# Performance work log

Measured on AMD Instinct MI355X. Metric: run time of the kernel, lower is better.

The kernel has to match this reference:

```python
import jax, jax.numpy as jnp
import numpy as np

B, N, E = 64, 128, 512
F_NODE, F_EDGE = 16, 8
NODE_SIZE = EDGE_SIZE = 64
NUM_STEPS, N_ITER, OMEGA = 3, 8, 0.75
CUTOFF, SMEAR, EPS = 50.0, -0.39, 1e-6


def mila(x):
    # mila with beta=-1: x * tanh(softplus(x - 1))
    return x * jnp.tanh(jax.nn.softplus(x - 1.0))


def ssp(x):
    return jax.nn.softplus(x) + 1e-3


def setup_inputs():
    key = jax.random.key(0)
    ks = iter(jax.random.split(key, 64))
    def nrm(shape, s=1.0):
        return jax.random.normal(next(ks), shape, jnp.float32) * s
    def he(shape):
        return nrm(shape, (2.0 / shape[-2]) ** 0.5)
    inp = {}
    inp['nodes1'] = nrm((N, F_NODE))
    inp['edges1'] = nrm((E, F_EDGE))
    inp['senders1'] = jax.random.randint(next(ks), (E,), 0, N)
    inp['receivers1'] = jax.random.randint(next(ks), (E,), 0, N)
    inp['nodes2'] = nrm((N, F_NODE))
    inp['edges2'] = nrm((E, F_EDGE))
    inp['senders2'] = jax.random.randint(next(ks), (E,), 0, N)
    inp['receivers2'] = jax.random.randint(next(ks), (E,), 0, N)
    c1 = jax.random.uniform(next(ks), (B, N, 3), jnp.float32, 0.0, 10.0)
    c2 = jax.random.uniform(next(ks), (B, N, 3), jnp.float32, 0.0, 10.0) + jnp.array([12.0, 0.0, 0.0])
    inp['coords1'], inp['coords2'] = c1, c2
    inp['distance_matrices'] = jnp.linalg.norm(c1[:, :, None, :] - c2[:, None, :, :], axis=-1)
    inp['multipoles'] = nrm((2, B, N, 1), 0.2)
    inp['W_emb_node'], inp['b_emb_node'] = he((F_NODE, NODE_SIZE)), jnp.zeros((NODE_SIZE,))
    inp['W_emb_edge'], inp['b_emb_edge'] = he((F_EDGE, EDGE_SIZE)), jnp.zeros((EDGE_SIZE,))
    inp['W_gn_edge'] = he((NUM_STEPS, EDGE_SIZE + 2 * NODE_SIZE, EDGE_SIZE))
    inp['b_gn_edge'] = jnp.zeros((NUM_STEPS, EDGE_SIZE))
    inp['W_gn_node'] = he((NUM_STEPS, NODE_SIZE + EDGE_SIZE, NODE_SIZE))
    inp['b_gn_node'] = jnp.zeros((NUM_STEPS, NODE_SIZE))
    inp['pp_W0'], inp['pp_b0'] = he((2 * NODE_SIZE, NODE_SIZE)), jnp.zeros((NODE_SIZE,))
    inp['pp_W1'], inp['pp_b1'] = he((NODE_SIZE, NODE_SIZE)), jnp.zeros((NODE_SIZE,))
    inp['pp_W2'], inp['pp_b2'] = he((NODE_SIZE, 5)), jnp.zeros((5,))
    inp['ap_W0'], inp['ap_b0'] = he((NODE_SIZE, NODE_SIZE)), jnp.zeros((NODE_SIZE,))
    inp['ap_W1'], inp['ap_b1'] = he((NODE_SIZE, NODE_SIZE)), jnp.zeros((NODE_SIZE,))
    inp['ap_W2'], inp['ap_b2'] = he((NODE_SIZE, 5)), jnp.zeros((5,))
    return inp


def _gnn(nodes, edges, senders, receivers, Wen, ben, Wee, bee, Wge, bge, Wgn, bgn):
    # GraphIndependent embedding, then NUM_STEPS InteractionNetwork blocks
    n = mila(nodes @ Wen + ben)
    e = mila(edges @ Wee + bee)
    for s in range(NUM_STEPS):
        e_in = jnp.concatenate([e, n[receivers], n[senders]], axis=-1)
        e = mila(e_in @ Wge[s] + bge[s])
        agg = jax.ops.segment_sum(e, receivers, num_segments=N)
        n = mila(jnp.concatenate([n, agg], axis=-1) @ Wgn[s] + bgn[s])
    return n


def _mlp3(x, W0, b0, W1, b1, W2, b2):
    h = mila(x @ W0 + b0)
    h = mila(h @ W1 + b1)
    return ssp(h @ W2 + b2)


def _induction(coords1, coords2, pol1, pol2, dist, q1, q2):
    # Thole-damped SCF induced dipoles between the two monomers
    r12 = coords1[:, :, None, :] - coords2[:, None, :, :]            # [B,N,N,3]
    R = dist[..., None]                                              # [B,N,N,1]
    R3 = R ** 3 + EPS
    au = jnp.sqrt(pol1[:, 0][:, None] * pol2[:, 0][None, :]) + EPS   # [N,N]
    u3 = dist ** 3 / au                                              # [B,N,N]
    exu = jnp.exp(SMEAR * u3)
    lam3 = (1.0 - exu)[..., None]
    lam5 = (1.0 - (1.0 - SMEAR * u3) * exu)[..., None]
    E0_1 = jnp.sum(q2[:, None, :, None] * lam3 * r12 / R3, axis=2)   # [B,N,3]
    E0_2 = jnp.sum(q1[:, :, None, None] * lam3 * (-r12) / R3, axis=1)
    eye = jnp.eye(3, dtype=coords1.dtype)
    T12 = (3.0 * lam5[..., None] * r12[..., :, None] * r12[..., None, :] / (R ** 5 + EPS)[..., None]
           - lam3[..., None] * eye / R3[..., None])                  # [B,N,N,3,3]
    p1, p2 = pol1[None], pol2[None]                                  # [1,N,1]
    mu1, mu2 = p1 * E0_1, p2 * E0_2
    def step(carry, _):
        m1, m2 = carry
        f1 = E0_1 + jnp.einsum('bijkl,bjl->bik', T12, m2)
        f2 = E0_2 + jnp.einsum('bijkl,bil->bjk', T12, m1)
        m1n = (1.0 - OMEGA) * m1 + OMEGA * p1 * f1
        m2n = (1.0 - OMEGA) * m2 + OMEGA * p2 * f2
        return (m1n, m2n), None
    (mu1, mu2), _ = jax.lax.scan(step, (mu1, mu2), None, length=N_ITER)
    energy = -0.5 * (jnp.sum(mu1 * E0_1, axis=(1, 2)) + jnp.sum(mu2 * E0_2, axis=(1, 2)))
    return energy, mu1, mu2


def _forward(nodes1, edges1, senders1, receivers1, nodes2, edges2, senders2, receivers2,
             coords1, coords2, multipoles, distance_matrices,
             W_emb_node, b_emb_node, W_emb_edge, b_emb_edge,
             W_gn_edge, b_gn_edge, W_gn_node, b_gn_node,
             pp_W0, pp_b0, pp_W1, pp_b1, pp_W2, pp_b2,
             ap_W0, ap_b0, ap_W1, ap_b1, ap_W2, ap_b2):
    Bsz = distance_matrices.shape[0]
    h1 = jnp.argmax(nodes1, axis=-1) == 0
    h2 = jnp.argmax(nodes2, axis=-1) == 0
    i1 = jnp.repeat(jnp.arange(N), N)
    i2 = jnp.tile(jnp.arange(N), N)
    R1 = distance_matrices.reshape(Bsz, -1, 1)                       # [B,P,1]
    R2 = R1 ** 2
    Rx1 = coords2[:, i2] - coords1[:, i1]                            # [B,P,3]
    # GNN embeddings (shared weights for both monomers)
    feats1 = _gnn(nodes1, edges1, senders1, receivers1, W_emb_node, b_emb_node,
                  W_emb_edge, b_emb_edge, W_gn_edge, b_gn_edge, W_gn_node, b_gn_node)
    feats2 = _gnn(nodes2, edges2, senders2, receivers2, W_emb_node, b_emb_node,
                  W_emb_edge, b_emb_edge, W_gn_edge, b_gn_edge, W_gn_node, b_gn_node)
    f1p, f2p = feats1[i1], feats2[i2]                                # [P,64]
    params = (_mlp3(jnp.concatenate([f1p, f2p], -1), pp_W0, pp_b0, pp_W1, pp_b1, pp_W2, pp_b2)
              + _mlp3(jnp.concatenate([f2p, f1p], -1), pp_W0, pp_b0, pp_W1, pp_b1, pp_W2, pp_b2))
    ap1 = _mlp3(feats1, ap_W0, ap_b0, ap_W1, ap_b1, ap_W2, ap_b2)    # [N,5]
    ap2 = _mlp3(feats2, ap_W0, ap_b0, ap_W1, ap_b1, ap_W2, ap_b2)
    a_d1, pol1, K1, dq1, a_e1 = jnp.split(ap1, 5, axis=-1)
    a_d2, pol2, K2, dq2, a_e2 = jnp.split(ap2, 5, axis=-1)
    q1, q2 = multipoles[0], multipoles[1]                            # [B,N,1]
    qe1 = jnp.where(h1[None, :, None], 1.0 - q1, 2.0 + dq1[None] - q1)
    qe2 = jnp.where(h2[None, :, None], 1.0 - q2, 2.0 + dq2[None] - q2)
    Rs = R1 + EPS
    B0 = 1.0 / Rs
    # induction (SCF) + charge transfer
    in_term, mu1, mu2 = _induction(coords1, coords2, pol1, pol2, distance_matrices,
                                   q1[..., 0], q2[..., 0])
    A_ct, b_ct = params[:, 3:4], params[:, 4:5]
    in_term = in_term - jnp.sum(A_ct[None] * jnp.exp(-b_ct[None] * R1), axis=(-1, -2))
    # BJ dispersion
    C6, C8, C10 = params[:, 0:1], params[:, 1:2], params[:, 2:3]
    r0_2 = C8 / (C6 + EPS)
    R6, R8, R10 = R2 ** 3, R2 ** 4, R2 ** 5
    bj = -(C6 / (R6 + r0_2 ** 3) + C8 / (R8 + r0_2 ** 4) + C10 / (R10 + r0_2 ** 5))
    disp_term = jnp.sum(jnp.where(R2 < CUTOFF ** 2, bj, 0.0), axis=(-1, -2))
    # damped charge-charge electrostatics
    q1p = jnp.take(q1, i1, axis=1)
    q2p = jnp.take(q2, i2, axis=1)
    bd = jnp.sqrt(a_d1[i1] * a_d2[i2])[None]                         # [1,P,1]
    fdamp = 1.0 - (1.0 + 0.5 * bd * R1) * jnp.exp(-bd * R1)
    es_term = jnp.sum(q1p * q2p * fdamp * B0, axis=(-1, -2))
    # anisotropic exchange (induced-dipole anisotropy along the pair axis)
    rhat = Rx1 * B0
    m1p = jnp.take(mu1, i1, axis=1)
    m2p = jnp.take(mu2, i2, axis=1)
    proj = jnp.sum((m1p - m2p) * rhat, axis=-1, keepdims=True)
    be = jnp.sqrt(a_e1[i1] * a_e2[i2])[None]
    Kp = (K1[i1] * K2[i2])[None]
    qe1p = jnp.take(qe1, i1, axis=1)
    qe2p = jnp.take(qe2, i2, axis=1)
    ex_term = jnp.sum(Kp * qe1p * qe2p * (1.0 + proj) * jnp.exp(-be * R1) * B0, axis=(-1, -2))
    total = ex_term + disp_term + es_term + in_term
    return total, es_term, in_term, ex_term, disp_term


def reference(nodes1, edges1, senders1, receivers1, nodes2, edges2, senders2, receivers2,
              coords1, coords2, multipoles, distance_matrices,
              W_emb_node, b_emb_node, W_emb_edge, b_emb_edge,
              W_gn_edge, b_gn_edge, W_gn_node, b_gn_node,
              pp_W0, pp_b0, pp_W1, pp_b1, pp_W2, pp_b2,
              ap_W0, ap_b0, ap_W1, ap_b1, ap_W2, ap_b2):
    return _forward(nodes1, edges1, senders1, receivers1, nodes2, edges2, senders2, receivers2,
                    coords1, coords2, multipoles, distance_matrices,
                    W_emb_node, b_emb_node, W_emb_edge, b_emb_edge,
                    W_gn_edge, b_gn_edge, W_gn_node, b_gn_node,
                    pp_W0, pp_b0, pp_W1, pp_b1, pp_W2, pp_b2,
                    ap_W0, ap_b0, ap_W1, ap_b1, ap_W2, ap_b2)
```

## Files before the change

kernel.cpp:

```cpp
#include <hip/hip_runtime.h>

#define DEVI __device__ __forceinline__

DEVI float b2f(unsigned short u){
  union { unsigned u; float f; } v; v.u = ((unsigned)u) << 16; return v.f;
}
DEVI unsigned short f2b(float f){
  union { float f; unsigned u; } v; v.f = f;
  unsigned r = (v.u + 0x7fffu + ((v.u >> 16) & 1u)) >> 16;
  return (unsigned short)r;
}
DEVI float splus(float x){ return fmaxf(x, 0.f) + log1pf(expf(-fabsf(x))); }
DEVI float mila(float x){ return x * tanhf(splus(x - 1.f)); }
DEVI float ssp_(float x){ return splus(x) + 0.001f; }
DEVI float rdist(const void* p, long idx, bool isbf){
  return isbf ? b2f(((const unsigned short*)p)[idx]) : ((const float*)p)[idx];
}

constexpr int OFF_N   = 0;
constexpr int OFF_E   = 16384;
constexpr int OFF_A1  = 81920;
constexpr int OFF_A2  = 90112;
constexpr int OFF_B1  = 98304;
constexpr int OFF_B2  = 106496;
constexpr int OFF_APT = 114688;
constexpr int OFF_HM  = 115968;
constexpr int OFF_PAR = 116224;
constexpr int OFF_MU1 = 198144;
constexpr int OFF_MU2 = 230912;
constexpr int OFF_ACC = 263680;
constexpr int OFF_FLAG= 263936;
constexpr int OFF_MIR = 264192;
constexpr int MTOT    = 162698;
constexpr int OFF_CNT = 3703696;
constexpr int OFF_LST = 3703952;

#define M_NODES1 (mir + 0)
#define M_EDGES1 (mir + 2048)
#define M_NODES2 (mir + 6144)
#define M_EDGES2 (mir + 8192)
#define M_C1     (mir + 12288)
#define M_C2     (mir + 36864)
#define M_MP     (mir + 61440)
#define M_WEN    (mir + 77824)
#define M_BEN    (mir + 78848)
#define M_WEE    (mir + 78912)
#define M_BEE    (mir + 79424)
#define M_WGE    (mir + 79488)
#define M_BGE    (mir + 116352)
#define M_WGN    (mir + 116544)
#define M_BGN    (mir + 141120)
#define M_PPW0   (mir + 141312)
#define M_PPB0   (mir + 149504)
#define M_PPW1   (mir + 149568)
#define M_PPB1   (mir + 153664)
#define M_PPW2   (mir + 153728)
#define M_PPB2   (mir + 154048)
#define M_APW0   (mir + 154053)
#define M_APB0   (mir + 158149)
#define M_APW1   (mir + 158213)
#define M_APB1   (mir + 162309)
#define M_APW2   (mir + 162373)
#define M_APB2   (mir + 162693)

__constant__ int c_moff[28] = {0,2048,6144,8192,12288,36864,61440,77824,
  78848,78912,79424,79488,116352,116544,141120,141312,149504,149568,
  153664,153728,154048,154053,158149,158213,162309,162373,162693,162698};
__constant__ int c_mcnt[27] = {2048,4096,2048,4096,24576,24576,16384,
  1024,64,512,64,36864,192,24576,192,8192,64,4096,64,320,5,4096,64,4096,64,320,5};

__global__ void __launch_bounds__(256) k_convert(
    const void* s0, const void* s1, const void* s2, const void* s3,
    const void* s4, const void* s5, const void* s6, const void* s7,
    const void* s8, const void* s9, const void* s10, const void* s11,
    const void* s12, const void* s13, const void* s14, const void* s15,
    const void* s16, const void* s17, const void* s18, const void* s19,
    const void* s20, const void* s21, const void* s22, const void* s23,
    const void* s24, const void* s25, const void* s26,
    const void* distraw, const int* recv1, const int* recv2, float* ws)
{
  __shared__ int sflag;
  __shared__ int bcnt[128];
  int t = threadIdx.x, bid = blockIdx.x;
  if (t < 64) {
    float v = b2f(((const unsigned short*)distraw)[t]);
    bool ok = (v > 0.25f) && (v < 512.f);
    unsigned long long m = __ballot(ok);
    if (t == 0) sflag = (m == ~0ull) ? 1 : 0;
  }
  __syncthreads();
  bool isbf = sflag != 0;
  if (bid < 636) {
    const void* sp[27] = {s0,s1,s2,s3,s4,s5,s6,s7,s8,s9,s10,s11,s12,s13,
                          s14,s15,s16,s17,s18,s19,s20,s21,s22,s23,s24,s25,s26};
    int g = bid*256 + t;
    if (g >= MTOT) return;
    int lo = 0, hi = 27;
    #pragma unroll
    for (int st = 0; st < 5; st++) {
      int mid = (lo + hi) >> 1;
      if (g >= c_moff[mid]) lo = mid; else hi = mid;
    }
    int local = g - c_moff[lo];
    if (local < c_mcnt[lo]) {
      float v = isbf ? b2f(((const unsigned short*)sp[lo])[local])
                     : ((const float*)sp[lo])[local];
      ws[OFF_MIR + g] = v;
    }
  } else if (bid < 956) {
    ws[OFF_PAR + (bid-636)*256 + t] = 0.f;
  } else if (bid == 956) {
    ws[OFF_ACC + t] = 0.f;
    if (t == 0) ws[OFF_FLAG] = isbf ? 1.f : 0.f;
  } else {
    int g = bid - 957;
    const int* recv = g ? recv2 : recv1;
    if (t < 128) bcnt[t] = 0;
    __syncthreads();
    for (int pass = 0; pass < 2; pass++) {
      int ed = pass*256 + t;
      int nd = recv[ed];
      int pos = atomicAdd(&bcnt[nd], 1);
      if (pos < 64) ((int*)ws)[OFF_LST + (g*128+nd)*64 + pos] = ed;
    }
    __syncthreads();
    if (t < 128) ((int*)ws)[OFF_CNT + g*128 + t] = bcnt[t];
  }
}

__global__ void __launch_bounds__(256) k_emb(float* ws)
{
  const float* mir = ws + OFF_MIR;
  int t = threadIdx.x, c = t & 63;
  int row = blockIdx.x * 4 + (t >> 6);
  if (row < 256) {
    int g = row >> 7, nd = row & 127;
    const float* src = g ? M_NODES2 : M_NODES1;
    float acc = M_BEN[c];
    for (int k = 0; k < 16; k++) acc += src[nd*16+k] * M_WEN[k*64+c];
    ws[OFF_N + (g*128+nd)*64 + c] = mila(acc);
  } else {
    int er = row - 256; int g = er >> 9, ed = er & 511;
    const float* src = g ? M_EDGES2 : M_EDGES1;
    float acc = M_BEE[c];
    for (int k = 0; k < 8; k++) acc += src[ed*8+k] * M_WEE[k*64+c];
    ws[OFF_E + (g*512+ed)*64 + c] = mila(acc);
  }
}

__global__ void __launch_bounds__(256) k_edge(const int* recv1, const int* send1,
    const int* recv2, const int* send2, int s, float* ws)
{
  const float* mir = ws + OFF_MIR;
  __shared__ float ein[4][192];
  int t = threadIdx.x;
  int le = t >> 6, c = t & 63;
  int eidx = blockIdx.x * 4;
  const float* n = ws + OFF_N;
  const float* e = ws + OFF_E;
  for (int q = t; q < 768; q += 256) {
    int ee = q / 192, k = q % 192;
    int ge = eidx + ee; int g = ge >> 9, ed = ge & 511;
    const int* recv = g ? recv2 : recv1;
    const int* send = g ? send2 : send1;
    float v;
    if (k < 64)       v = e[(g*512+ed)*64 + k];
    else if (k < 128) v = n[(g*128+recv[ed])*64 + (k-64)];
    else              v = n[(g*128+send[ed])*64 + (k-128)];
    ein[ee][k] = v;
  }
  __syncthreads();
  const float* W = M_WGE + s*192*64;
  float acc = M_BGE[s*64+c];
  for (int k = 0; k < 192; k++) acc += ein[le][k] * W[k*64+c];
  int ge = eidx + le; int g = ge >> 9, ed = ge & 511;
  ws[OFF_E + (g*512+ed)*64 + c] = mila(acc);
}

__global__ void __launch_bounds__(64) k_node(const int* recv1, const int* recv2,
    int s, float* ws)
{
  const float* mir = ws + OFF_MIR;
  __shared__ float xin[128];
  int c = threadIdx.x;
  int g = blockIdx.x >> 7, nd = blockIdx.x & 127;
  const float* n = ws + OFF_N;
  const float* e = ws + OFF_E;
  int cnt = ((const int*)ws)[OFF_CNT + g*128 + nd];
  float agg = 0.f;
  if (cnt <= 64) {
    const int* lst = (const int*)ws + OFF_LST + (g*128+nd)*64;
    for (int q = 0; q < cnt; q++) {
      int ed = lst[q];
      agg += e[(g*512+ed)*64 + c];
    }
  } else {
    const int* recv = g ? recv2 : recv1;
    for (int ed = 0; ed < 512; ed++)
      if (recv[ed] == nd) agg += e[(g*512+ed)*64 + c];
  }
  xin[c] = n[(g*128+nd)*64 + c];
  xin[64 + c] = agg;
  __syncthreads();
  const float* W = M_WGN + s*128*64;
  float acc = M_BGN[s*64+c];
  for (int k = 0; k < 128; k++) acc += xin[k] * W[k*64+c];
  ws[OFF_N + (g*128+nd)*64 + c] = mila(acc);
}

__global__ void __launch_bounds__(256) k_prep(float* ws)
{
  const float* mir = ws + OFF_MIR;
  __shared__ float sh[4][64], sh2[4][64];
  int t = threadIdx.x;
  const float* n = ws + OFF_N;
  if (blockIdx.x < 128) {
    int T = blockIdx.x >> 5, rg = blockIdx.x & 31;
    int r = rg*4 + (t >> 6), c = t & 63;
    const float* f = (T == 0 || T == 2) ? n : (n + 128*64);
    int wofs = (T == 0 || T == 3) ? 0 : 64;
    float acc = (T == 1 || T == 2) ? M_PPB0[c] : 0.f;
    for (int k = 0; k < 64; k++) acc += f[r*64+k] * M_PPW0[(wofs+k)*64 + c];
    if (T == 0)      ws[OFF_A1 + r*64 + c] = acc;
    else if (T == 1) ws[OFF_A2 + c*128 + r] = acc;
    else if (T == 2) ws[OFF_B1 + r*64 + c] = acc;
    else             ws[OFF_B2 + c*128 + r] = acc;
  } else {
    int b2i = blockIdx.x - 128;
    int g = b2i >> 5, grp = b2i & 31;
    int ln = t >> 6, c = t & 63;
    int nd = grp*4 + ln;
    const float* f = n + (g*128+nd)*64;
    float acc = M_APB0[c];
    for (int k = 0; k < 64; k++) acc += f[k] * M_APW0[k*64+c];
    sh[ln][c] = mila(acc);
    __syncthreads();
    acc = M_APB1[c];
    for (int k = 0; k < 64; k++) acc += sh[ln][k] * M_APW1[k*64+c];
    sh2[ln][c] = mila(acc);
    __syncthreads();
    if (c < 5) {
      float a2 = M_APB2[c];
      for (int k = 0; k < 64; k++) a2 += sh2[ln][k] * M_APW2[k*5+c];
      ws[OFF_APT + (g*5+c)*128 + nd] = ssp_(a2);
    }
    if (c == 0) {
      const float* ns = (g ? M_NODES2 : M_NODES1) + nd*16;
      float v0 = ns[0];
      float ok = 1.f;
      for (int k = 1; k < 16; k++) if (ns[k] > v0) ok = 0.f;
      ws[OFF_HM + g*128 + nd] = ok;
    }
  }
}

__global__ void __launch_bounds__(256) k_pair(float* ws)
{
  const float* mir = ws + OFF_MIR;
  float* params = ws + OFF_PAR;
  __shared__ float W1s[4096];
  __shared__ float W2s[320];
  __shared__ float b1s[64], b2s[8], bases[64];
  __shared__ float h0s[4096];
  __shared__ float opart[64][4][5];
  int t = threadIdx.x;
  int jl = t & 63, h = t >> 6;
  int i = blockIdx.x >> 2, dir = (blockIdx.x >> 1) & 1, jh = blockIdx.x & 1;
  const float* base = ws + (dir ? OFF_B1 : OFF_A1) + i*64;
  const float* oT   = ws + (dir ? OFF_B2 : OFF_A2) + jh*64;
  #pragma unroll
  for (int q = 0; q < 16; q++) W1s[q*256 + t] = M_PPW1[q*256 + t];
  for (int q = t; q < 320; q += 256) W2s[q] = M_PPW2[q];
  if (t < 64) { b1s[t] = M_PPB1[t]; bases[t] = base[t]; }
  if (t >= 64 && t < 72) b2s[t-64] = (t-64 < 5) ? M_PPB2[t-64] : 0.f;
  __syncthreads();
  #pragma unroll
  for (int q = 0; q < 16; q++) {
    int idx = q*256 + t;
    int c = idx >> 6, j2 = idx & 63;
    h0s[idx] = mila(bases[c] + oT[c*128 + j2]);
  }
  __syncthreads();
  float h1c[16];
  #pragma unroll
  for (int k = 0; k < 16; k++) h1c[k] = b1s[h*16 + k];
  for (int c = 0; c < 64; c++) {
    float h0c = h0s[c*64 + jl];
    const float4* w4 = (const float4*)&W1s[c*64 + h*16];
    float4 wa = w4[0], wb = w4[1], wc = w4[2], wd = w4[3];
    h1c[0]  += h0c*wa.x; h1c[1]  += h0c*wa.y; h1c[2]  += h0c*wa.z; h1c[3]  += h0c*wa.w;
    h1c[4]  += h0c*wb.x; h1c[5]  += h0c*wb.y; h1c[6]  += h0c*wb.z; h1c[7]  += h0c*wb.w;
    h1c[8]  += h0c*wc.x; h1c[9]  += h0c*wc.y; h1c[10] += h0c*wc.z; h1c[11] += h0c*wc.w;
    h1c[12] += h0c*wd.x; h1c[13] += h0c*wd.y; h1c[14] += h0c*wd.z; h1c[15] += h0c*wd.w;
  }
  float o5p[5] = {0.f, 0.f, 0.f, 0.f, 0.f};
  #pragma unroll
  for (int k = 0; k < 16; k++) {
    float hk = mila(h1c[k]);
    int kk = h*16 + k;
    #pragma unroll
    for (int o = 0; o < 5; o++) o5p[o] += hk * W2s[kk*5 + o];
  }
  #pragma unroll
  for (int o = 0; o < 5; o++) opart[jl][h][o] = o5p[o];
  __syncthreads();
  if (t < 64) {
    int p = i*128 + jh*64 + t;
    #pragma unroll
    for (int o = 0; o < 5; o++) {
      float val = b2s[o] + opart[t][0][o] + opart[t][1][o]
                         + opart[t][2][o] + opart[t][3][o];
      atomicAdd(&params[p*5 + o], ssp_(val));
    }
  }
}

__global__ void __launch_bounds__(1024) k_ind_all(const void* distp, float* ws)
{
  const float* mir = ws + OFF_MIR;
  const float* apT = ws + OFF_APT;
  __shared__ __align__(8) float2 sC35[128*132];
  __shared__ float4 c1s[128], c2s[128], m1s[128], m2s[128];
  __shared__ float4 e01s[128], e02s[128], f1s[128], f2s[128];
  __shared__ float p1s[128], p2s[128], q1s[128], q2s[128];
  __shared__ float esum[128];
  int b = blockIdx.x, t = threadIdx.x;
  bool isbf = ws[OFF_FLAG] != 0.f;
  if (t < 128) {
    c1s[t] = make_float4(M_C1[(b*128+t)*3], M_C1[(b*128+t)*3+1], M_C1[(b*128+t)*3+2], 0.f);
    c2s[t] = make_float4(M_C2[(b*128+t)*3], M_C2[(b*128+t)*3+1], M_C2[(b*128+t)*3+2], 0.f);
    p1s[t] = apT[128 + t];
    p2s[t] = apT[(5+1)*128 + t];
    q1s[t] = M_MP[b*128 + t];
    q2s[t] = M_MP[8192 + b*128 + t];
  }
  __syncthreads();
  int il = t >> 3, sub = t & 7;
  {
    float4 c1 = c1s[il];
    float p1 = p1s[il];
    float ex = 0, ey = 0, ez = 0;
    #pragma unroll 4
    for (int jj = 0; jj < 16; jj++) {
      int j = sub + 8*jj;
      float R = rdist(distp, (long)b*16384 + il*128 + j, isbf);
      float R2 = R*R, R3 = R2*R, R5 = R3*R2;
      float au = sqrtf(p1 * p2s[j]) + 1e-6f;
      float u3 = R3 / au;
      float exu = expf(-0.39f * u3);
      float c3 = (1.f - exu) / (R3 + 1e-6f);
      float c5 = 3.f * (1.f - (1.f + 0.39f*u3) * exu) / (R5 + 1e-6f);
      sC35[il*132 + j] = make_float2(c3, c5);
      float w = q2s[j] * c3;
      ex += w*(c1.x - c2s[j].x); ey += w*(c1.y - c2s[j].y); ez += w*(c1.z - c2s[j].z);
    }
    #pragma unroll
    for (int m = 1; m <= 4; m <<= 1) {
      ex += __shfl_xor(ex, m, 64); ey += __shfl_xor(ey, m, 64); ez += __shfl_xor(ez, m, 64);
    }
    if (sub == 0) e01s[il] = make_float4(ex, ey, ez, 0.f);
  }
  __syncthreads();
  {
    float4 c2 = c2s[il];
    float ex = 0, ey = 0, ez = 0;
    #pragma unroll 4
    for (int jj = 0; jj < 16; jj++) {
      int i = sub + 8*jj;
      float c3 = sC35[i*132 + il].x;
      float w = q1s[i] * c3;
      ex -= w*(c1s[i].x - c2.x); ey -= w*(c1s[i].y - c2.y); ez -= w*(c1s[i].z - c2.z);
    }
    #pragma unroll
    for (int m = 1; m <= 4; m <<= 1) {
      ex += __shfl_xor(ex, m, 64); ey += __shfl_xor(ey, m, 64); ez += __shfl_xor(ez, m, 64);
    }
    if (sub == 0) e02s[il] = make_float4(ex, ey, ez, 0.f);
  }
  __syncthreads();
  if (t < 128) {
    float4 e1 = e01s[t], e2 = e02s[t];
    m1s[t] = make_float4(p1s[t]*e1.x, p1s[t]*e1.y, p1s[t]*e1.z, 0.f);
    m2s[t] = make_float4(p2s[t]*e2.x, p2s[t]*e2.y, p2s[t]*e2.z, 0.f);
  }
  __syncthreads();
  for (int it = 0; it < 8; it++) {
    {
      float4 c1 = c1s[il];
      float fx = 0, fy = 0, fz = 0;
      #pragma unroll 4
      for (int jj = 0; jj < 16; jj++) {
        int j = sub + 8*jj;
        float2 cc = sC35[il*132 + j];
        float4 m2 = m2s[j], c2 = c2s[j];
        float rx = c1.x - c2.x, ry = c1.y - c2.y, rz = c1.z - c2.z;
        float dot = rx*m2.x + ry*m2.y + rz*m2.z;
        float a = cc.y * dot;
        fx += a*rx - cc.x*m2.x; fy += a*ry - cc.x*m2.y; fz += a*rz - cc.x*m2.z;
      }
      #pragma unroll
      for (int m = 1; m <= 4; m <<= 1) {
        fx += __shfl_xor(fx, m, 64); fy += __shfl_xor(fy, m, 64); fz += __shfl_xor(fz, m, 64);
      }
      if (sub == 0) f1s[il] = make_float4(fx, fy, fz, 0.f);
    }
    {
      float4 c2 = c2s[il];
      float fx = 0, fy = 0, fz = 0;
      #pragma unroll 4
      for (int jj = 0; jj < 16; jj++) {
        int i = sub + 8*jj;
        float2 cc = sC35[i*132 + il];
        float4 m1 = m1s[i], c1 = c1s[i];
        float rx = c1.x - c2.x, ry = c1.y - c2.y, rz = c1.z - c2.z;
        float dot = rx*m1.x + ry*m1.y + rz*m1.z;
        float a = cc.y * dot;
        fx += a*rx - cc.x*m1.x; fy += a*ry - cc.x*m1.y; fz += a*rz - cc.x*m1.z;
      }
      #pragma unroll
      for (int m = 1; m <= 4; m <<= 1) {
        fx += __shfl_xor(fx, m, 64); fy += __shfl_xor(fy, m, 64); fz += __shfl_xor(fz, m, 64);
      }
      if (sub == 0) f2s[il] = make_float4(fx, fy, fz, 0.f);
    }
    __syncthreads();
    if (t < 128) {
      float4 f1 = f1s[t], e1 = e01s[t], mo1 = m1s[t];
      float4 f2 = f2s[t], e2 = e02s[t], mo2 = m2s[t];
      float p1 = p1s[t], p2 = p2s[t];
      m1s[t] = make_float4(0.25f*mo1.x + 0.75f*p1*(e1.x + f1.x),
                           0.25f*mo1.y + 0.75f*p1*(e1.y + f1.y),
                           0.25f*mo1.z + 0.75f*p1*(e1.z + f1.z), 0.f);
      m2s[t] = make_float4(0.25f*mo2.x + 0.75f*p2*(e2.x + f2.x),
                           0.25f*mo2.y + 0.75f*p2*(e2.y + f2.y),
                           0.25f*mo2.z + 0.75f*p2*(e2.z + f2.z), 0.f);
    }
    __syncthreads();
  }
  if (t < 128) {
    float4 m1 = m1s[t], m2 = m2s[t], e1 = e01s[t], e2 = e02s[t];
    esum[t] = m1.x*e1.x + m1.y*e1.y + m1.z*e1.z
            + m2.x*e2.x + m2.y*e2.y + m2.z*e2.z;
    *(float4*)&ws[OFF_MU1 + (b*128+t)*4] = m1;
    *(float4*)&ws[OFF_MU2 + (b*128+t)*4] = m2;
  }
  __syncthreads();
  if (t == 0) {
    float s = 0.f;
    for (int k = 0; k < 128; k++) s += esum[k];
    ws[OFF_ACC + 64 + b] = -0.5f * s;
  }
}

__global__ void __launch_bounds__(256) k_terms(const void* distp, float* ws)
{
  const float* mir = ws + OFF_MIR;
  int b = blockIdx.x >> 2, q = blockIdx.x & 3;
  int t = threadIdx.x;
  bool isbf = ws[OFF_FLAG] != 0.f;
  const float* par = ws + OFF_PAR;
  const float* apT = ws + OFF_APT;
  const float* hm  = ws + OFF_HM;
  const float* mu1 = ws + OFF_MU1;
  const float* mu2 = ws + OFF_MU2;
  float es = 0, ct = 0, ex = 0, dp = 0;
  for (int s = 0; s < 16; s++) {
    int p = q*4096 + s*256 + t;
    int i = p >> 7, j = p & 127;
    float C6 = par[p*5+0], C8 = par[p*5+1], C10 = par[p*5+2];
    float Act = par[p*5+3], bct = par[p*5+4];
    float R = rdist(distp, (long)b*16384 + p, isbf);
    float Rs = R + 1e-6f;
    float B0 = 1.f / Rs;
    float R2 = R*R;
    float R6 = R2*R2*R2, R8 = R6*R2, R10 = R8*R2;
    float r0 = C8 / (C6 + 1e-6f);
    float D6 = r0*r0*r0, D8 = D6*r0, D10 = D8*r0;
    if (R2 < 2500.f) dp -= C6/(R6+D6) + C8/(R8+D8) + C10/(R10+D10);
    ct += Act * expf(-bct * R);
    float q1v = M_MP[b*128 + i];
    float q2v = M_MP[8192 + b*128 + j];
    float ad1 = apT[0*128 + i],   ad2 = apT[(5+0)*128 + j];
    float k1v = apT[2*128 + i],   k2v = apT[(5+2)*128 + j];
    float ae1 = apT[4*128 + i],   ae2 = apT[(5+4)*128 + j];
    float dq1 = apT[3*128 + i],   dq2 = apT[(5+3)*128 + j];
    float bd = sqrtf(ad1*ad2), be = sqrtf(ae1*ae2), Kp = k1v*k2v;
    float ebd = expf(-bd * R);
    float fd = 1.f - (1.f + 0.5f*bd*R) * ebd;
    es += q1v * q2v * fd * B0;
    float rxx = M_C2[(b*128+j)*3+0] - M_C1[(b*128+i)*3+0];
    float rxy = M_C2[(b*128+j)*3+1] - M_C1[(b*128+i)*3+1];
    float rxz = M_C2[(b*128+j)*3+2] - M_C1[(b*128+i)*3+2];
    float m1x = mu1[(b*128+i)*4+0], m1y = mu1[(b*128+i)*4+1], m1z = mu1[(b*128+i)*4+2];
    float m2x = mu2[(b*128+j)*4+0], m2y = mu2[(b*128+j)*4+1], m2z = mu2[(b*128+j)*4+2];
    float proj = ((m1x-m2x)*rxx + (m1y-m2y)*rxy + (m1z-m2z)*rxz) * B0;
    float h1v = hm[i], h2v = hm[128 + j];
    float qe1 = h1v > 0.5f ? (1.f - q1v) : (2.f + dq1 - q1v);
    float qe2 = h2v > 0.5f ? (1.f - q2v) : (2.f + dq2 - q2v);
    ex += Kp * qe1 * qe2 * (1.f + proj) * expf(-be * R) * B0;
  }
  __shared__ float sred[4][4];
  for (int m = 32; m >= 1; m >>= 1) {
    es += __shfl_xor(es, m, 64); ct += __shfl_xor(ct, m, 64);
    ex += __shfl_xor(ex, m, 64); dp += __shfl_xor(dp, m, 64);
  }
  int w = t >> 6;
  if ((t & 63) == 0) { sred[w][0] = es; sred[w][1] = ct; sred[w][2] = ex; sred[w][3] = dp; }
  __syncthreads();
  if (t == 0) {
    float a0 = 0, a1 = 0, a2 = 0, a3 = 0;
    for (int ww = 0; ww < 4; ww++) { a0 += sred[ww][0]; a1 += sred[ww][1]; a2 += sred[ww][2]; a3 += sred[ww][3]; }
    atomicAdd(&ws[OFF_ACC +   0 + b], a0);
    atomicAdd(&ws[OFF_ACC +  64 + b], -a1);
    atomicAdd(&ws[OFF_ACC + 128 + b], a2);
    atomicAdd(&ws[OFF_ACC + 192 + b], a3);
  }
}

__global__ void __launch_bounds__(64) k_total(const float* ws, void* outv)
{
  int b = threadIdx.x;
  float es  = ws[OFF_ACC +   0 + b];
  float inv = ws[OFF_ACC +  64 + b];
  float ex  = ws[OFF_ACC + 128 + b];
  float dp  = ws[OFF_ACC + 192 + b];
  float tot = ex + dp + es + inv;
  if (ws[OFF_FLAG] != 0.f) {
    unsigned short* out = (unsigned short*)outv;
    out[b]       = f2b(tot);
    out[64 + b]  = f2b(es);
    out[128 + b] = f2b(inv);
    out[192 + b] = f2b(ex);
    out[256 + b] = f2b(dp);
  } else {
    float* out = (float*)outv;
    out[b]       = tot;
    out[64 + b]  = es;
    out[128 + b] = inv;
    out[192 + b] = ex;
    out[256 + b] = dp;
  }
}

extern "C" void kernel_launch(void* const* d_in, const int* in_sizes, int n_in,
                              void* d_out, int out_size, void* d_ws, size_t ws_size,
                              hipStream_t stream)
{
  const int* send1 = (const int*)d_in[2];
  const int* recv1 = (const int*)d_in[3];
  const int* send2 = (const int*)d_in[6];
  const int* recv2 = (const int*)d_in[7];
  float* ws = (float*)d_ws;

  k_convert<<<959, 256, 0, stream>>>(
      d_in[0], d_in[1], d_in[4], d_in[5], d_in[8], d_in[9], d_in[11],
      d_in[12], d_in[13], d_in[14], d_in[15], d_in[16], d_in[17], d_in[18],
      d_in[19], d_in[20], d_in[21], d_in[22], d_in[23], d_in[24], d_in[25],
      d_in[26], d_in[27], d_in[28], d_in[29], d_in[30], d_in[31],
      d_in[10], recv1, recv2, ws);

  k_emb<<<320, 256, 0, stream>>>(ws);
  for (int s = 0; s < 3; s++) {
    k_edge<<<256, 256, 0, stream>>>(recv1, send1, recv2, send2, s, ws);
    k_node<<<256, 64, 0, stream>>>(recv1, recv2, s, ws);
  }
  k_prep<<<192, 256, 0, stream>>>(ws);
  k_pair<<<512, 256, 0, stream>>>(ws);
  k_ind_all<<<64, 1024, 0, stream>>>(d_in[10], ws);
  k_terms<<<256, 256, 0, stream>>>(d_in[10], ws);
  k_total<<<1, 64, 0, stream>>>(ws, d_out);
}
```

Before: 294.2 us.

## Shrink induction block to 256 threads with 4 rows per thread; widen k_terms grid

The induction kernel drops from 1024 to 256 threads per block, and each thread now handles four rows/columns, keeping coordinates and polarizabilities in registers. This reuses the shared-memory loads of the j-side data across rows and reduces barrier cost across the 8 iterations. The downside is less parallelism per block with only 64 blocks. Separately, k_terms is split over 1024 blocks instead of 256, each doing 4 strides instead of 16, to fill more CUs. That split may add more partial-sum atomics or writes at the end.

```diff
diff --git a/kernel.cpp b/kernel.cpp
--- a/kernel.cpp
+++ b/kernel.cpp
@@ -315,7 +315,7 @@
   }
 }
 
-__global__ void __launch_bounds__(1024) k_ind_all(const void* distp, float* ws)
+__global__ void __launch_bounds__(256) k_ind_all(const void* distp, float* ws)
 {
   const float* mir = ws + OFF_MIR;
   const float* apT = ws + OFF_APT;
@@ -336,46 +336,80 @@
   }
   __syncthreads();
   int il = t >> 3, sub = t & 7;
+  float4 c1r[4], c2c[4];
+  float p1r[4];
+  #pragma unroll
+  for (int k = 0; k < 4; k++) {
+    c1r[k] = c1s[il + 32*k];
+    c2c[k] = c2s[il + 32*k];
+    p1r[k] = p1s[il + 32*k];
+  }
   {
-    float4 c1 = c1s[il];
-    float p1 = p1s[il];
-    float ex = 0, ey = 0, ez = 0;
-    #pragma unroll 4
+    float e1a[4][3] = {{0,0,0},{0,0,0},{0,0,0},{0,0,0}};
     for (int jj = 0; jj < 16; jj++) {
       int j = sub + 8*jj;
-      float R = rdist(distp, (long)b*16384 + il*128 + j, isbf);
-      float R2 = R*R, R3 = R2*R, R5 = R3*R2;
-      float au = sqrtf(p1 * p2s[j]) + 1e-6f;
-      float u3 = R3 / au;
-      float exu = expf(-0.39f * u3);
-      float c3 = (1.f - exu) / (R3 + 1e-6f);
-      float c5 = 3.f * (1.f - (1.f + 0.39f*u3) * exu) / (R5 + 1e-6f);
-      sC35[il*132 + j] = make_float2(c3, c5);
-      float w = q2s[j] * c3;
-      ex += w*(c1.x - c2s[j].x); ey += w*(c1.y - c2s[j].y); ez += w*(c1.z - c2s[j].z);
+      float p2j = p2s[j], q2j = q2s[j];
+      float4 c2 = c2s[j];
+      #pragma unroll
+      for (int k = 0; k < 4; k++) {
+        int i = il + 32*k;
+        float R = rdist(distp, (long)b*16384 + i*128 + j, isbf);
+        float R2 = R*R, R3 = R2*R, R5 = R3*R2;
+        float au = sqrtf(p1r[k] * p2j) + 1e-6f;
+        float u3 = R3 / au;
+        float exu = expf(-0.39f * u3);
+        float c3 = (1.f - exu) / (R3 + 1e-6f);
+        float c5 = 3.f * (1.f - (1.f + 0.39f*u3) * exu) / (R5 + 1e-6f);
+        sC35[i*132 + j] = make_float2(c3, c5);
+        float w = q2j * c3;
+        e1a[k][0] += w*(c1r[k].x - c2.x);
+        e1a[k][1] += w*(c1r[k].y - c2.y);
+        e1a[k][2] += w*(c1r[k].z - c2.z);
+      }
     }
     #pragma unroll
-    for (int m = 1; m <= 4; m <<= 1) {
-      ex += __shfl_xor(ex, m, 64); ey += __shfl_xor(ey, m, 64); ez += __shfl_xor(ez, m, 64);
-    }
-    if (sub == 0) e01s[il] = make_float4(ex, ey, ez, 0.f);
+    for (int k = 0; k < 4; k++)
+      #pragma unroll
+      for (int m = 1; m <= 4; m <<= 1) {
+        e1a[k][0] += __shfl_xor(e1a[k][0], m, 64);
+        e1a[k][1] += __shfl_xor(e1a[k][1], m, 64);
+        e1a[k][2] += __shfl_xor(e1a[k][2], m, 64);
+      }
+    if (sub == 0) {
+      #pragma unroll
+      for (int k = 0; k < 4; k++)
+        e01s[il + 32*k] = make_float4(e1a[k][0], e1a[k][1], e1a[k][2], 0.f);
+    }
   }
   __syncthreads();
   {
-    float4 c2 = c2s[il];
-    float ex = 0, ey = 0, ez = 0;
-    #pragma unroll 4
+    float e2a[4][3] = {{0,0,0},{0,0,0},{0,0,0},{0,0,0}};
     for (int jj = 0; jj < 16; jj++) {
       int i = sub + 8*jj;
-      float c3 = sC35[i*132 + il].x;
-      float w = q1s[i] * c3;
-      ex -= w*(c1s[i].x - c2.x); ey -= w*(c1s[i].y - c2.y); ez -= w*(c1s[i].z - c2.z);
+      float4 c1 = c1s[i];
+      float q1i = q1s[i];
+      #pragma unroll
+      for (int k = 0; k < 4; k++) {
+        float c3 = sC35[i*132 + il + 32*k].x;
+        float w = q1i * c3;
+        e2a[k][0] -= w*(c1.x - c2c[k].x);
+        e2a[k][1] -= w*(c1.y - c2c[k].y);
+        e2a[k][2] -= w*(c1.z - c2c[k].z);
+      }
     }
     #pragma unroll
-    for (int m = 1; m <= 4; m <<= 1) {
-      ex += __shfl_xor(ex, m, 64); ey += __shfl_xor(ey, m, 64); ez += __shfl_xor(ez, m, 64);
-    }
-    if (sub == 0) e02s[il] = make_float4(ex, ey, ez, 0.f);
+    for (int k = 0; k < 4; k++)
+      #pragma unroll
+      for (int m = 1; m <= 4; m <<= 1) {
+        e2a[k][0] += __shfl_xor(e2a[k][0], m, 64);
+        e2a[k][1] += __shfl_xor(e2a[k][1], m, 64);
+        e2a[k][2] += __shfl_xor(e2a[k][2], m, 64);
+      }
+    if (sub == 0) {
+      #pragma unroll
+      for (int k = 0; k < 4; k++)
+        e02s[il + 32*k] = make_float4(e2a[k][0], e2a[k][1], e2a[k][2], 0.f);
+    }
   }
   __syncthreads();
   if (t < 128) {
@@ -386,42 +420,64 @@
   __syncthreads();
   for (int it = 0; it < 8; it++) {
     {
-      float4 c1 = c1s[il];
-      float fx = 0, fy = 0, fz = 0;
-      #pragma unroll 4
+      float fa[4][3] = {{0,0,0},{0,0,0},{0,0,0},{0,0,0}};
       for (int jj = 0; jj < 16; jj++) {
         int j = sub + 8*jj;
-        float2 cc = sC35[il*132 + j];
         float4 m2 = m2s[j], c2 = c2s[j];
-        float rx = c1.x - c2.x, ry = c1.y - c2.y, rz = c1.z - c2.z;
-        float dot = rx*m2.x + ry*m2.y + rz*m2.z;
-        float a = cc.y * dot;
-        fx += a*rx - cc.x*m2.x; fy += a*ry - cc.x*m2.y; fz += a*rz - cc.x*m2.z;
-      }
-      #pragma unroll
-      for (int m = 1; m <= 4; m <<= 1) {
-        fx += __shfl_xor(fx, m, 64); fy += __shfl_xor(fy, m, 64); fz += __shfl_xor(fz, m, 64);
-      }
-      if (sub == 0) f1s[il] = make_float4(fx, fy, fz, 0.f);
+        #pragma unroll
+        for (int k = 0; k < 4; k++) {
+          float2 cc = sC35[(il + 32*k)*132 + j];
+          float rx = c1r[k].x - c2.x, ry = c1r[k].y - c2.y, rz = c1r[k].z - c2.z;
+          float dot = rx*m2.x + ry*m2.y + rz*m2.z;
+          float a = cc.y * dot;
+          fa[k][0] += a*rx - cc.x*m2.x;
+          fa[k][1] += a*ry - cc.x*m2.y;
+          fa[k][2] += a*rz - cc.x*m2.z;
+        }
+      }
+      #pragma unroll
+      for (int k = 0; k < 4; k++)
+        #pragma unroll
+        for (int m = 1; m <= 4; m <<= 1) {
+          fa[k][0] += __shfl_xor(fa[k][0], m, 64);
+          fa[k][1] += __shfl_xor(fa[k][1], m, 64);
+          fa[k][2] += __shfl_xor(fa[k][2], m, 64);
+        }
+      if (sub == 0) {
+        #pragma unroll
+        for (int k = 0; k < 4; k++)
+          f1s[il + 32*k] = make_float4(fa[k][0], fa[k][1], fa[k][2], 0.f);
+      }
     }
     {
-      float4 c2 = c2s[il];
-      float fx = 0, fy = 0, fz = 0;
-      #pragma unroll 4
+      float fa[4][3] = {{0,0,0},{0,0,0},{0,0,0},{0,0,0}};
       for (int jj = 0; jj < 16; jj++) {
         int i = sub + 8*jj;
-        float2 cc = sC35[i*132 + il];
         float4 m1 = m1s[i], c1 = c1s[i];
-        float rx = c1.x - c2.x, ry = c1.y - c2.y, rz = c1.z - c2.z;
-        float dot = rx*m1.x + ry*m1.y + rz*m1.z;
-        float a = cc.y * dot;
-        fx += a*rx - cc.x*m1.x; fy += a*ry - cc.x*m1.y; fz += a*rz - cc.x*m1.z;
-      }
-      #pragma unroll
-      for (int m = 1; m <= 4; m <<= 1) {
-        fx += __shfl_xor(fx, m, 64); fy += __shfl_xor(fy, m, 64); fz += __shfl_xor(fz, m, 64);
-      }
-      if (sub == 0) f2s[il] = make_float4(fx, fy, fz, 0.f);
+        #pragma unroll
+        for (int k = 0; k < 4; k++) {
+          float2 cc = sC35[i*132 + il + 32*k];
+          float rx = c1.x - c2c[k].x, ry = c1.y - c2c[k].y, rz = c1.z - c2c[k].z;
+          float dot = rx*m1.x + ry*m1.y + rz*m1.z;
+          float a = cc.y * dot;
+          fa[k][0] += a*rx - cc.x*m1.x;
+          fa[k][1] += a*ry - cc.x*m1.y;
+          fa[k][2] += a*rz - cc.x*m1.z;
+        }
+      }
+      #pragma unroll
+      for (int k = 0; k < 4; k++)
+        #pragma unroll
+        for (int m = 1; m <= 4; m <<= 1) {
+          fa[k][0] += __shfl_xor(fa[k][0], m, 64);
+          fa[k][1] += __shfl_xor(fa[k][1], m, 64);
+          fa[k][2] += __shfl_xor(fa[k][2], m, 64);
+        }
+      if (sub == 0) {
+        #pragma unroll
+        for (int k = 0; k < 4; k++)
+          f2s[il + 32*k] = make_float4(fa[k][0], fa[k][1], fa[k][2], 0.f);
+      }
     }
     __syncthreads();
     if (t < 128) {
@@ -455,7 +511,7 @@
 __global__ void __launch_bounds__(256) k_terms(const void* distp, float* ws)
 {
   const float* mir = ws + OFF_MIR;
-  int b = blockIdx.x >> 2, q = blockIdx.x & 3;
+  int b = blockIdx.x >> 4, q = blockIdx.x & 15;
   int t = threadIdx.x;
   bool isbf = ws[OFF_FLAG] != 0.f;
   const float* par = ws + OFF_PAR;
@@ -464,8 +520,8 @@
   const float* mu1 = ws + OFF_MU1;
   const float* mu2 = ws + OFF_MU2;
   float es = 0, ct = 0, ex = 0, dp = 0;
-  for (int s = 0; s < 16; s++) {
-    int p = q*4096 + s*256 + t;
+  for (int s = 0; s < 4; s++) {
+    int p = q*1024 + s*256 + t;
     int i = p >> 7, j = p & 127;
     float C6 = par[p*5+0], C8 = par[p*5+1], C10 = par[p*5+2];
     float Act = par[p*5+3], bct = par[p*5+4];
@@ -566,7 +622,7 @@
   }
   k_prep<<<192, 256, 0, stream>>>(ws);
   k_pair<<<512, 256, 0, stream>>>(ws);
-  k_ind_all<<<64, 1024, 0, stream>>>(d_in[10], ws);
-  k_terms<<<256, 256, 0, stream>>>(d_in[10], ws);
+  k_ind_all<<<64, 256, 0, stream>>>(d_in[10], ws);
+  k_terms<<<1024, 256, 0, stream>>>(d_in[10], ws);
   k_total<<<1, 64, 0, stream>>>(ws, d_out);
 }
```

Measured after the change: 299.1 us. Within noise of the previous version (+1.7%).

## Split induction iteration across two thread groups and widen k_terms grid

Applied to the files above, without the earlier changes.

The 1024-thread induction kernel now has half of the threads compute the field on molecule 1 while the other half compute it on molecule 2, each thread handling two rows. The coordinates each thread reuses are hoisted into registers before the 8-iteration loop, which replaces two sequential passes per iteration with one concurrent pass. Separately, k_terms now launches 1024 blocks of 4 strips each instead of 256 blocks of 16 strips, to raise occupancy. The cost is more register pressure in the induction kernel and four times as many partial results to reduce in k_terms, which must be handled in the code not shown.

```diff
diff --git a/kernel.cpp b/kernel.cpp
--- a/kernel.cpp
+++ b/kernel.cpp
@@ -384,44 +384,75 @@
     m2s[t] = make_float4(p2s[t]*e2.x, p2s[t]*e2.y, p2s[t]*e2.z, 0.f);
   }
   __syncthreads();
+  int grp = t >> 9;
+  int tl = t & 511;
+  int il2 = tl >> 3, sub2 = tl & 7;
+  int r0 = il2, r1 = il2 + 64;
+  float hx[16], hy[16], hz[16];
+  #pragma unroll
+  for (int jj = 0; jj < 16; jj++) {
+    int o = sub2 + 8*jj;
+    float4 v = grp ? c1s[o] : c2s[o];
+    hx[jj] = v.x; hy[jj] = v.y; hz[jj] = v.z;
+  }
+  float4 cA = grp ? c2s[r0] : c1s[r0];
+  float4 cB = grp ? c2s[r1] : c1s[r1];
   for (int it = 0; it < 8; it++) {
-    {
-      float4 c1 = c1s[il];
-      float fx = 0, fy = 0, fz = 0;
-      #pragma unroll 4
+    float fax = 0, fay = 0, faz = 0, fbx = 0, fby = 0, fbz = 0;
+    if (grp == 0) {
+      #pragma unroll
       for (int jj = 0; jj < 16; jj++) {
-        int j = sub + 8*jj;
-        float2 cc = sC35[il*132 + j];
-        float4 m2 = m2s[j], c2 = c2s[j];
-        float rx = c1.x - c2.x, ry = c1.y - c2.y, rz = c1.z - c2.z;
-        float dot = rx*m2.x + ry*m2.y + rz*m2.z;
-        float a = cc.y * dot;
-        fx += a*rx - cc.x*m2.x; fy += a*ry - cc.x*m2.y; fz += a*rz - cc.x*m2.z;
+        int j = sub2 + 8*jj;
+        float2 cca = sC35[r0*132 + j];
+        float2 ccb = sC35[r1*132 + j];
+        float4 m2 = m2s[j];
+        {
+          float rx = cA.x - hx[jj], ry = cA.y - hy[jj], rz = cA.z - hz[jj];
+          float dot = rx*m2.x + ry*m2.y + rz*m2.z;
+          float a = cca.y * dot;
+          fax += a*rx - cca.x*m2.x; fay += a*ry - cca.x*m2.y; faz += a*rz - cca.x*m2.z;
+        }
+        {
+          float rx = cB.x - hx[jj], ry = cB.y - hy[jj], rz = cB.z - hz[jj];
+          float dot = rx*m2.x + ry*m2.y + rz*m2.z;
+          float a = ccb.y * dot;
+          fbx += a*rx - ccb.x*m2.x; fby += a*ry - ccb.x*m2.y; fbz += a*rz - ccb.x*m2.z;
+        }
       }
+    } else {
       #pragma unroll
-      for (int m = 1; m <= 4; m <<= 1) {
-        fx += __shfl_xor(fx, m, 64); fy += __shfl_xor(fy, m, 64); fz += __shfl_xor(fz, m, 64);
+      for (int jj = 0; jj < 16; jj++) {
+        int i = sub2 + 8*jj;
+        float2 cca = sC35[i*132 + r0];
+        float2 ccb = sC35[i*132 + r1];
+        float4 m1 = m1s[i];
+        {
+          float rx = hx[jj] - cA.x, ry = hy[jj] - cA.y, rz = hz[jj] - cA.z;
+          float dot = rx*m1.x + ry*m1.y + rz*m1.z;
+          float a = cca.y * dot;
+          fax += a*rx - cca.x*m1.x; fay += a*ry - cca.x*m1.y; faz += a*rz - cca.x*m1.z;
+        }
+        {
+          float rx = hx[jj] - cB.x, ry = hy[jj] - cB.y, rz = hz[jj] - cB.z;
+          float dot = rx*m1.x + ry*m1.y + rz*m1.z;
+          float a = ccb.y * dot;
+          fbx += a*rx - ccb.x*m1.x; fby += a*ry - ccb.x*m1.y; fbz += a*rz - ccb.x*m1.z;
+        }
       }
-      if (sub == 0) f1s[il] = make_float4(fx, fy, fz, 0.f);
-    }
-    {
-      float4 c2 = c2s[il];
-      float fx = 0, fy = 0, fz = 0;
-      #pragma unroll 4
-      for (int jj = 0; jj < 16; jj++) {
-        int i = sub + 8*jj;
-        float2 cc = sC35[i*132 + il];
-        float4 m1 = m1s[i], c1 = c1s[i];
-        float rx = c1.x - c2.x, ry = c1.y - c2.y, rz = c1.z - c2.z;
-        float dot = rx*m1.x + ry*m1.y + rz*m1.z;
-        float a = cc.y * dot;
-        fx += a*rx - cc.x*m1.x; fy += a*ry - cc.x*m1.y; fz += a*rz - cc.x*m1.z;
+    }
+    #pragma unroll
+    for (int m = 1; m <= 4; m <<= 1) {
+      fax += __shfl_xor(fax, m, 64); fay += __shfl_xor(fay, m, 64); faz += __shfl_xor(faz, m, 64);
+      fbx += __shfl_xor(fbx, m, 64); fby += __shfl_xor(fby, m, 64); fbz += __shfl_xor(fbz, m, 64);
+    }
+    if (sub2 == 0) {
+      if (grp == 0) {
+        f1s[r0] = make_float4(fax, fay, faz, 0.f);
+        f1s[r1] = make_float4(fbx, fby, fbz, 0.f);
+      } else {
+        f2s[r0] = make_float4(fax, fay, faz, 0.f);
+        f2s[r1] = make_float4(fbx, fby, fbz, 0.f);
       }
-      #pragma unroll
-      for (int m = 1; m <= 4; m <<= 1) {
-        fx += __shfl_xor(fx, m, 64); fy += __shfl_xor(fy, m, 64); fz += __shfl_xor(fz, m, 64);
-      }
-      if (sub == 0) f2s[il] = make_float4(fx, fy, fz, 0.f);
     }
     __syncthreads();
     if (t < 128) {
@@ -455,7 +486,7 @@
 __global__ void __launch_bounds__(256) k_terms(const void* distp, float* ws)
 {
   const float* mir = ws + OFF_MIR;
-  int b = blockIdx.x >> 2, q = blockIdx.x & 3;
+  int b = blockIdx.x >> 4, q = blockIdx.x & 15;
   int t = threadIdx.x;
   bool isbf = ws[OFF_FLAG] != 0.f;
   const float* par = ws + OFF_PAR;
@@ -464,8 +495,8 @@
   const float* mu1 = ws + OFF_MU1;
   const float* mu2 = ws + OFF_MU2;
   float es = 0, ct = 0, ex = 0, dp = 0;
-  for (int s = 0; s < 16; s++) {
-    int p = q*4096 + s*256 + t;
+  for (int s = 0; s < 4; s++) {
+    int p = q*1024 + s*256 + t;
     int i = p >> 7, j = p & 127;
     float C6 = par[p*5+0], C8 = par[p*5+1], C10 = par[p*5+2];
     float Act = par[p*5+3], bct = par[p*5+4];
@@ -567,6 +598,6 @@
   k_prep<<<192, 256, 0, stream>>>(ws);
   k_pair<<<512, 256, 0, stream>>>(ws);
   k_ind_all<<<64, 1024, 0, stream>>>(d_in[10], ws);
-  k_terms<<<256, 256, 0, stream>>>(d_in[10], ws);
+  k_terms<<<1024, 256, 0, stream>>>(d_in[10], ws);
   k_total<<<1, 64, 0, stream>>>(ws, d_out);
 }
```

After: 398.4 us. 1.35x slower.
